# Kernel optimization log

Measured on AMD Instinct MI355X. Metric: run time of the kernel, lower is better.

The kernel has to match this reference:

```python
import jax, jax.numpy as jnp
import numpy as np
from jax import lax

# dims
B, T = 64, 1024
ANNOT, RNN, MEM, ATTN = 512, 1024, 512, 512
FILTERS, KSIZE = 32, 31
PAD = (KSIZE - 1) // 2  # 15, SAME padding


def setup_inputs() -> dict:
    key = jax.random.key(0)
    ks = jax.random.split(key, 20)
    s = 0.02
    return {
        "memory": jax.random.normal(ks[0], (B, MEM), jnp.float32),
        "context": jax.random.normal(ks[1], (B, ANNOT), jnp.float32),
        "rnn_state": jax.random.normal(ks[2], (B, RNN), jnp.float32),
        "annots": jax.random.normal(ks[3], (B, T, ANNOT), jnp.float32),
        "atten": jax.random.uniform(ks[4], (B, 2, T), jnp.float32),
        "mask": jnp.ones((B, T), jnp.int32),
        "t": 0,
        # GRUCell params (torch gate order: r, z, n)
        "W_ih": jax.random.normal(ks[5], (3 * RNN, ANNOT + MEM), jnp.float32) * s,
        "W_hh": jax.random.normal(ks[6], (3 * RNN, RNN), jnp.float32) * s,
        "b_ih": jnp.zeros((3 * RNN,), jnp.float32),
        "b_hh": jnp.zeros((3 * RNN,), jnp.float32),
        # location-sensitive attention params
        "conv_w": jax.random.normal(ks[7], (FILTERS, 2, KSIZE), jnp.float32) * s,
        "loc_w": jax.random.normal(ks[8], (ATTN, FILTERS), jnp.float32) * s,
        "loc_b": jnp.zeros((ATTN,), jnp.float32),
        "q_w": jax.random.normal(ks[9], (ATTN, RNN), jnp.float32) * s,
        "q_b": jnp.zeros((ATTN,), jnp.float32),
        "a_w": jax.random.normal(ks[10], (ATTN, ANNOT), jnp.float32) * s,
        "a_b": jnp.zeros((ATTN,), jnp.float32),
        "v_w": jax.random.normal(ks[11], (1, ATTN), jnp.float32) * s,
    }


def _gru_cell(x, h, W_ih, W_hh, b_ih, b_hh):
    gi = x @ W_ih.T + b_ih  # [B, 3H]
    gh = h @ W_hh.T + b_hh
    i_r, i_z, i_n = jnp.split(gi, 3, axis=-1)
    h_r, h_z, h_n = jnp.split(gh, 3, axis=-1)
    r = jax.nn.sigmoid(i_r + h_r)
    z = jax.nn.sigmoid(i_z + h_z)
    n = jnp.tanh(i_n + r * h_n)
    return (1.0 - z) * n + z * h


def reference(memory, context, rnn_state, annots, atten, mask, t,
              W_ih, W_hh, b_ih, b_hh, conv_w, loc_w, loc_b,
              q_w, q_b, a_w, a_b, v_w):
    # GRU step on [memory; prev_context]
    rnn_input = jnp.concatenate([memory, context], axis=-1)  # [B, MEM+ANNOT]
    rnn_output = _gru_cell(rnn_input, rnn_state, W_ih, W_hh, b_ih, b_hh)  # [B, RNN]

    # location features: SAME conv over [B, 2, T] -> [B, FILTERS, T]
    loc_conv = lax.conv_general_dilated(
        atten, conv_w, window_strides=(1,), padding=[(PAD, PAD)],
        dimension_numbers=("NCH", "OIH", "NCH"))
    processed_loc = jnp.einsum("bft,af->bta", loc_conv, loc_w) + loc_b  # [B,T,ATTN]

    processed_query = (rnn_output @ q_w.T + q_b)[:, None, :]            # [B,1,ATTN]
    processed_annots = jnp.einsum("btd,ad->bta", annots, a_w) + a_b     # [B,T,ATTN]

    energy = jnp.tanh(processed_query + processed_annots + processed_loc)
    alignment = jnp.einsum("bta,a->bt", energy, v_w[0])                 # [B,T]

    # mask fill with -inf where mask == 0
    alignment = jnp.where(mask == 0, -jnp.inf, alignment)

    # sigmoid-normalized attention weights
    sig = jax.nn.sigmoid(alignment)
    alignment = sig / jnp.sum(sig, axis=1, keepdims=True)               # [B,T]

    new_context = jnp.einsum("bt,btd->bd", alignment, annots)           # [B,ANNOT]
    return rnn_output, new_context, alignment
```

## Files before the change

kernel.cpp:

```cpp
#include <hip/hip_runtime.h>

typedef float f32x4 __attribute__((ext_vector_type(4)));
typedef short bf16x8 __attribute__((ext_vector_type(8)));

__device__ __forceinline__ unsigned int pk2(float a, float b) {
    unsigned int ua = __float_as_uint(a); ua += 0x7FFFu + ((ua >> 16) & 1u);
    unsigned int ub = __float_as_uint(b); ub += 0x7FFFu + ((ub >> 16) & 1u);
    return __builtin_amdgcn_perm(ub, ua, 0x07060302u);
}
__device__ __forceinline__ unsigned short bf16_rne(float a) {
    unsigned int ua = __float_as_uint(a);
    ua += 0x7FFFu + ((ua >> 16) & 1u);
    return (unsigned short)(ua >> 16);
}
__device__ __forceinline__ float tanh_fast(float x) {
    float e = __expf(x + x);
    return 1.f - 2.f / (e + 1.f);
}
__device__ __forceinline__ f32x4 mfma16(bf16x8 a, bf16x8 b, f32x4 c) {
    return __builtin_amdgcn_mfma_f32_16x16x32_bf16(a, b, c, 0, 0, 0);
}
__device__ __forceinline__ void ald16(const void* g, void* l) {
    __builtin_amdgcn_global_load_lds(
        (const __attribute__((address_space(1))) unsigned int*)g,
        (__attribute__((address_space(3))) unsigned int*)l, 16, 0, 0);
}

#define Q_WIH   786432
#define Q_WHH   1572864
#define Q_QW    1703936
#define Q_X2    1720320
#define Q_X1    1736704
#define Q_BAW   1802240
#define Q_BLW   1806336
#define Q_EB    1806464
#define NCVT    7057

__global__ __launch_bounds__(256) void k_prep(
    const float* __restrict__ Wih, const float* __restrict__ Whh,
    const float* __restrict__ qw, const float* __restrict__ rnn_state,
    const float* __restrict__ memory, const float* __restrict__ context,
    const float* __restrict__ aw, const float* __restrict__ lw,
    const float* __restrict__ ab, const float* __restrict__ lb,
    const float* __restrict__ atten, const float* __restrict__ convw,
    unsigned short* __restrict__ Wihb, unsigned short* __restrict__ Whhb,
    unsigned short* __restrict__ qwb, unsigned short* __restrict__ X2b,
    unsigned short* __restrict__ X1b, unsigned short* __restrict__ Bbig,
    float* __restrict__ ebias, unsigned short* __restrict__ Lconv)
{
    __shared__ float att_s[2 * 160];
    __shared__ float cw_s[1984];
    const int tid = threadIdx.x;
    if (blockIdx.x < NCVT) {
        int q = blockIdx.x * 256 + tid;
        if (q >= Q_EB) return;
        if (q < Q_WIH) {
            int i = q * 4;
            float4 v = *(const float4*)(Wih + i);
            uint2 u; u.x = pk2(v.x, v.y); u.y = pk2(v.z, v.w);
            *(uint2*)(Wihb + i) = u;
        } else if (q < Q_WHH) {
            int i = (q - Q_WIH) * 4;
            float4 v = *(const float4*)(Whh + i);
            uint2 u; u.x = pk2(v.x, v.y); u.y = pk2(v.z, v.w);
            *(uint2*)(Whhb + i) = u;
        } else if (q < Q_QW) {
            int i = (q - Q_WHH) * 4;
            float4 v = *(const float4*)(qw + i);
            uint2 u; u.x = pk2(v.x, v.y); u.y = pk2(v.z, v.w);
            *(uint2*)(qwb + i) = u;
        } else if (q < Q_X2) {
            int i = (q - Q_QW) * 4;
            float4 v = *(const float4*)(rnn_state + i);
            uint2 u; u.x = pk2(v.x, v.y); u.y = pk2(v.z, v.w);
            *(uint2*)(X2b + i) = u;
        } else if (q < Q_X1) {
            int i = (q - Q_X2) * 4;
            int b = i >> 10, c = i & 1023;
            const float* s = (c < 512) ? (memory + b * 512 + c) : (context + b * 512 + (c - 512));
            float4 v = *(const float4*)s;
            uint2 u; u.x = pk2(v.x, v.y); u.y = pk2(v.z, v.w);
            *(uint2*)(X1b + i) = u;
        } else if (q < Q_BAW) {
            int i = (q - Q_X1) * 4;
            int a = i >> 9, c = i & 511;
            float4 v = *(const float4*)(aw + a * 512 + c);
            uint2 u; u.x = pk2(v.x, v.y); u.y = pk2(v.z, v.w);
            *(uint2*)(Bbig + a * 544 + c) = u;
        } else if (q < Q_BLW) {
            int i = (q - Q_BAW) * 4;
            int a = i >> 5, c = i & 31;
            float4 v = *(const float4*)(lw + a * 32 + c);
            uint2 u; u.x = pk2(v.x, v.y); u.y = pk2(v.z, v.w);
            *(uint2*)(Bbig + a * 544 + 512 + c) = u;
        } else {
            int i = (q - Q_BLW) * 4;
            float4 va = *(const float4*)(ab + i);
            float4 vb = *(const float4*)(lb + i);
            float4 r; r.x = va.x + vb.x; r.y = va.y + vb.y; r.z = va.z + vb.z; r.w = va.w + vb.w;
            *(float4*)(ebias + i) = r;
        }
    } else {
        const int bid = blockIdx.x - NCVT;
        const int b = bid >> 3;
        const int tbase = (bid & 7) * 128;
        for (int i = tid; i < 320; i += 256) {
            int c = i / 160, j = i % 160;
            float v = 0.f;
            int pos = tbase - 15 + j;
            if (j < 158 && pos >= 0 && pos < 1024) v = atten[b * 2048 + c * 1024 + pos];
            att_s[c * 160 + j] = v;
        }
        for (int i = tid; i < 1984; i += 256) cw_s[i] = convw[i];
        __syncthreads();
        const int f = tid & 31, tq = tid >> 5;
        float acc[16];
#pragma unroll
        for (int i = 0; i < 16; ++i) acc[i] = 0.f;
        for (int c = 0; c < 2; ++c) {
            for (int k = 0; k < 31; ++k) {
                float w = cw_s[f * 62 + c * 31 + k];
                int base = c * 160 + tq * 16 + k;
#pragma unroll
                for (int ti = 0; ti < 16; ++ti) acc[ti] += w * att_s[base + ti];
            }
        }
#pragma unroll
        for (int ti = 0; ti < 16; ++ti) {
            int t = tbase + tq * 16 + ti;
            Lconv[(b * 1024 + t) * 32 + f] = bf16_rne(acc[ti]);
        }
    }
}

__global__ __launch_bounds__(256, 4) void k_gemm_ks(
    const unsigned short* __restrict__ A1, const unsigned short* __restrict__ A2,
    const unsigned short* __restrict__ B1, const unsigned short* __restrict__ B2,
    float* __restrict__ C, int N, int nTiles, int n_split, int K, int Klen)
{
    __shared__ __align__(16) unsigned short As[64 * 32];
    __shared__ __align__(16) unsigned short Bs[128 * 32];
    const int tid = threadIdx.x;
    const int nb = blockIdx.x % nTiles;
    const int ks = blockIdx.x / nTiles;
    const int nBase = nb * 128;
    const bool use2 = nBase >= n_split;
    const unsigned short* A = use2 ? A2 : A1;
    const unsigned short* B = use2 ? B2 : B1;
    const int brow0 = nBase - (use2 ? n_split : 0);
    const int lane = tid & 63, w = tid >> 6;
    const int c = lane & 15, qd = lane >> 4;
    const int lr = lane >> 2;
    const int swzl = ((lane & 3) ^ ((lr >> 1) & 3)) * 8;

    const f32x4 fz = {0.f, 0.f, 0.f, 0.f};
    f32x4 acc[4][2];
#pragma unroll
    for (int i = 0; i < 4; ++i) { acc[i][0] = fz; acc[i][1] = fz; }

    const int k0b = ks * Klen;
    const int nkc = Klen >> 5;
    for (int kc = 0; kc < nkc; ++kc) {
        const int k0 = k0b + kc * 32;
        ald16(A + (size_t)(w * 16 + lr) * K + k0 + swzl, &As[w * 512]);
        ald16(B + (size_t)(brow0 + w * 16 + lr) * K + k0 + swzl, &Bs[w * 512]);
        ald16(B + (size_t)(brow0 + 64 + w * 16 + lr) * K + k0 + swzl, &Bs[2048 + w * 512]);
        __syncthreads();
        const int rdoff = (qd ^ ((c >> 1) & 3)) * 8;
        bf16x8 af[4];
#pragma unroll
        for (int i = 0; i < 4; ++i) af[i] = *(const bf16x8*)&As[(i * 16 + c) * 32 + rdoff];
#pragma unroll
        for (int j = 0; j < 2; ++j) {
            bf16x8 bj = *(const bf16x8*)&Bs[(w * 32 + j * 16 + c) * 32 + rdoff];
#pragma unroll
            for (int i = 0; i < 4; ++i) acc[i][j] = mfma16(af[i], bj, acc[i][j]);
        }
        __syncthreads();
    }
    float* Cp = C + (size_t)ks * 64 * N;
#pragma unroll
    for (int i = 0; i < 4; ++i)
#pragma unroll
        for (int r = 0; r < 4; ++r) {
            int row = i * 16 + qd * 4 + r;
#pragma unroll
            for (int j = 0; j < 2; ++j) {
                int col = nBase + w * 32 + j * 16 + c;
                Cp[row * N + col] = acc[i][j][r];
            }
        }
}

__global__ __launch_bounds__(256) void k_gates(
    const float* __restrict__ Cg, const float* __restrict__ h0,
    const float* __restrict__ bih, const float* __restrict__ bhh,
    float* __restrict__ outv, unsigned short* __restrict__ X3b)
{
    int idx = blockIdx.x * 256 + threadIdx.x;
    int b = idx >> 10, h = idx & 1023;
    const float* g0 = Cg + b * 6144;
    const float* g1 = Cg + 393216 + b * 6144;
    float ir = g0[h] + g1[h] + bih[h];
    float iz = g0[h + 1024] + g1[h + 1024] + bih[h + 1024];
    float inn = g0[h + 2048] + g1[h + 2048] + bih[h + 2048];
    float hr = g0[h + 3072] + g1[h + 3072] + bhh[h];
    float hz = g0[h + 4096] + g1[h + 4096] + bhh[h + 1024];
    float hn = g0[h + 5120] + g1[h + 5120] + bhh[h + 2048];
    float r = 1.f / (1.f + __expf(-(ir + hr)));
    float z = 1.f / (1.f + __expf(-(iz + hz)));
    float n = tanh_fast(inn + r * hn);
    float o = (1.f - z) * n + z * h0[idx];
    outv[idx] = o;
    X3b[idx] = bf16_rne(o);
}

__global__ __launch_bounds__(256, 2) void k_attn(
    const float* __restrict__ annots, const unsigned short* __restrict__ Lconv,
    const unsigned short* __restrict__ Bbig, const float* __restrict__ pqP,
    const float* __restrict__ qb, const float* __restrict__ ebias,
    const float* __restrict__ vw, float* __restrict__ wsal)
{
    __shared__ __align__(16) unsigned short As[2][64 * 32];
    __shared__ __align__(16) unsigned short Bs[2][512 * 32];
    __shared__ float red[4][64];
    const int tid = threadIdx.x;
    const int btBase = blockIdx.x * 64;
    const int b = btBase >> 10;
    const int lane = tid & 63, w = tid >> 6;
    const int c = lane & 15, qd = lane >> 4;
    const int lr = lane >> 2;
    const int swzl = ((lane & 3) ^ ((lr >> 1) & 3)) * 8;
    const int arow = tid >> 2, alc = tid & 3;
    const int apofs = (alc ^ ((arow >> 1) & 3)) * 8;

    const f32x4 fz = {0.f, 0.f, 0.f, 0.f};
    f32x4 acc[4][8];
#pragma unroll
    for (int i = 0; i < 4; ++i)
#pragma unroll
        for (int j = 0; j < 8; ++j) acc[i][j] = fz;

    const float* aP = annots + (size_t)(btBase + arow) * 512 + alc * 8;
    const unsigned short* bP = Bbig + (size_t)(w * 16 + lr) * 544 + swzl;

#pragma unroll
    for (int s = 0; s < 8; ++s)
        ald16(bP + (size_t)s * 64 * 544, &Bs[0][s * 2048 + w * 512]);
    {
        float4 v0 = *(const float4*)(aP);
        float4 v1 = *(const float4*)(aP + 4);
        uint4 u;
        u.x = pk2(v0.x, v0.y); u.y = pk2(v0.z, v0.w);
        u.z = pk2(v1.x, v1.y); u.w = pk2(v1.z, v1.w);
        *(uint4*)&As[0][arow * 32 + apofs] = u;
    }
    __syncthreads();

    for (int kc = 0; kc < 17; ++kc) {
        const int cur = kc & 1, nxt = cur ^ 1;
        float4 v0n, v1n;
        if (kc < 16) {
            const int k1 = (kc + 1) * 32;
#pragma unroll
            for (int s = 0; s < 8; ++s)
                ald16(bP + (size_t)s * 64 * 544 + k1, &Bs[nxt][s * 2048 + w * 512]);
            if (kc < 15) {
                v0n = *(const float4*)(aP + k1);
                v1n = *(const float4*)(aP + k1 + 4);
            } else {
                ald16(Lconv + (size_t)(btBase + w * 16 + lr) * 32 + swzl, &As[nxt][w * 512]);
            }
        }
        const int rdoff = (qd ^ ((c >> 1) & 3)) * 8;
        bf16x8 af[4];
#pragma unroll
        for (int i = 0; i < 4; ++i) af[i] = *(const bf16x8*)&As[cur][(i * 16 + c) * 32 + rdoff];
        __builtin_amdgcn_s_setprio(1);
#pragma unroll
        for (int j = 0; j < 8; ++j) {
            bf16x8 bj = *(const bf16x8*)&Bs[cur][(w * 128 + j * 16 + c) * 32 + rdoff];
#pragma unroll
            for (int i = 0; i < 4; ++i) acc[i][j] = mfma16(af[i], bj, acc[i][j]);
        }
        __builtin_amdgcn_s_setprio(0);
        if (kc < 16) {
            if (kc < 15) {
                uint4 u;
                u.x = pk2(v0n.x, v0n.y); u.y = pk2(v0n.z, v0n.w);
                u.z = pk2(v1n.x, v1n.y); u.w = pk2(v1n.z, v1n.w);
                *(uint4*)&As[nxt][arow * 32 + apofs] = u;
            }
            __syncthreads();
        }
    }
    float pe[8], vv[8];
#pragma unroll
    for (int j = 0; j < 8; ++j) {
        int colg = w * 128 + j * 16 + c;
        pe[j] = pqP[b * 512 + colg] + pqP[32768 + b * 512 + colg] + qb[colg] + ebias[colg];
        vv[j] = vw[colg];
    }
#pragma unroll
    for (int i = 0; i < 4; ++i)
#pragma unroll
        for (int r = 0; r < 4; ++r) {
            float p = 0.f;
#pragma unroll
            for (int j = 0; j < 8; ++j)
                p += vv[j] * tanh_fast(acc[i][j][r] + pe[j]);
            p += __shfl_xor(p, 1);
            p += __shfl_xor(p, 2);
            p += __shfl_xor(p, 4);
            p += __shfl_xor(p, 8);
            if (c == 0) red[w][i * 16 + qd * 4 + r] = p;
        }
    __syncthreads();
    if (tid < 64)
        wsal[btBase + tid] = red[0][tid] + red[1][tid] + red[2][tid] + red[3][tid];
}

__global__ __launch_bounds__(256) void k_ctxA(
    const float* __restrict__ annots, const float* __restrict__ wsal,
    const int* __restrict__ mask, float* __restrict__ ctxP)
{
    __shared__ float cx[4][512];
    const int b = blockIdx.x >> 3;
    const int tc = blockIdx.x & 7;
    const int tid = threadIdx.x, lane = tid & 63, wv = tid >> 6;
    const int t0 = tc * 128 + wv * 32;
    const float* wp = wsal + b * 1024;
    const int* mp = mask + b * 1024;
    const float* ap = annots + (size_t)(b * 1024 + t0) * 512 + lane * 4;

    float a0 = 0.f, a1 = 0.f, a2 = 0.f, a3 = 0.f;
    float a4 = 0.f, a5 = 0.f, a6 = 0.f, a7 = 0.f;
#pragma unroll 4
    for (int r = 0; r < 32; ++r) {
        int t = t0 + r;
        float raw = wp[t];
        float s = (mp[t] != 0) ? 1.f / (1.f + __expf(-raw)) : 0.f;
        float4 va = *(const float4*)(ap + (size_t)r * 512);
        float4 vb = *(const float4*)(ap + (size_t)r * 512 + 256);
        a0 += s * va.x; a1 += s * va.y; a2 += s * va.z; a3 += s * va.w;
        a4 += s * vb.x; a5 += s * vb.y; a6 += s * vb.z; a7 += s * vb.w;
    }
    cx[wv][lane * 4 + 0] = a0; cx[wv][lane * 4 + 1] = a1;
    cx[wv][lane * 4 + 2] = a2; cx[wv][lane * 4 + 3] = a3;
    cx[wv][256 + lane * 4 + 0] = a4; cx[wv][256 + lane * 4 + 1] = a5;
    cx[wv][256 + lane * 4 + 2] = a6; cx[wv][256 + lane * 4 + 3] = a7;
    __syncthreads();
    float* cp = ctxP + (size_t)(tc * 64 + b) * 512;
    cp[tid]       = cx[0][tid]       + cx[1][tid]       + cx[2][tid]       + cx[3][tid];
    cp[tid + 256] = cx[0][tid + 256] + cx[1][tid + 256] + cx[2][tid + 256] + cx[3][tid + 256];
}

__global__ __launch_bounds__(256) void k_ctxB(
    const float* __restrict__ wsal, const int* __restrict__ mask,
    const float* __restrict__ ctxP, float* __restrict__ out)
{
    __shared__ float sv[1024];
    __shared__ float wsum[4];
    const int b = blockIdx.x;
    const int tid = threadIdx.x;
    float lsum = 0.f;
#pragma unroll
    for (int p = 0; p < 4; ++p) {
        int t = p * 256 + tid;
        int bt = b * 1024 + t;
        float raw = wsal[bt];
        float s = (mask[bt] != 0) ? 1.f / (1.f + __expf(-raw)) : 0.f;
        sv[t] = s;
        lsum += s;
    }
    for (int off = 32; off > 0; off >>= 1) lsum += __shfl_xor(lsum, off);
    if ((tid & 63) == 0) wsum[tid >> 6] = lsum;
    __syncthreads();
    const float tot = wsum[0] + wsum[1] + wsum[2] + wsum[3];
    const float inv = 1.f / tot;
#pragma unroll
    for (int p = 0; p < 4; ++p) {
        int t = p * 256 + tid;
        out[98304 + b * 1024 + t] = sv[t] * inv;
    }
#pragma unroll
    for (int h = 0; h < 2; ++h) {
        int d = h * 256 + tid;
        float csum = 0.f;
#pragma unroll
        for (int tc = 0; tc < 8; ++tc)
            csum += ctxP[(size_t)(tc * 64 + b) * 512 + d];
        out[65536 + b * 512 + d] = csum * inv;
    }
}

extern "C" void kernel_launch(void* const* d_in, const int* in_sizes, int n_in,
                              void* d_out, int out_size, void* d_ws, size_t ws_size,
                              hipStream_t stream) {
    const float* memory    = (const float*)d_in[0];
    const float* context   = (const float*)d_in[1];
    const float* rnn_state = (const float*)d_in[2];
    const float* annots    = (const float*)d_in[3];
    const float* atten     = (const float*)d_in[4];
    const int*   mask      = (const int*)d_in[5];
    const float* W_ih   = (const float*)d_in[7];
    const float* W_hh   = (const float*)d_in[8];
    const float* b_ih   = (const float*)d_in[9];
    const float* b_hh   = (const float*)d_in[10];
    const float* conv_w = (const float*)d_in[11];
    const float* loc_w  = (const float*)d_in[12];
    const float* loc_b  = (const float*)d_in[13];
    const float* q_w    = (const float*)d_in[14];
    const float* q_b    = (const float*)d_in[15];
    const float* a_w    = (const float*)d_in[16];
    const float* a_b    = (const float*)d_in[17];
    const float* v_w    = (const float*)d_in[18];
    float* out = (float*)d_out;

    char* w8 = (char*)d_ws;
    unsigned short* Lconv = (unsigned short*)(w8 + 0);
    unsigned short* Bbig  = (unsigned short*)(w8 + 4194304);
    unsigned short* Wihb  = (unsigned short*)(w8 + 4751360);
    unsigned short* Whhb  = (unsigned short*)(w8 + 11042816);
    unsigned short* qwb   = (unsigned short*)(w8 + 17334272);
    unsigned short* X1b   = (unsigned short*)(w8 + 18382848);
    unsigned short* X2b   = (unsigned short*)(w8 + 18513920);
    unsigned short* X3b   = (unsigned short*)(w8 + 18644992);
    float*          Cgru  = (float*)(w8 + 18776064);
    float*          pqP   = (float*)(w8 + 18776064);
    float*          ctxP  = (float*)(w8 + 18776064);
    float*          wsal  = (float*)(w8 + 19824640);
    float*          ebias = (float*)(w8 + 21921792);

    k_prep<<<NCVT + 512, 256, 0, stream>>>(W_ih, W_hh, q_w, rnn_state, memory, context,
                                           a_w, loc_w, a_b, loc_b, atten, conv_w,
                                           Wihb, Whhb, qwb, X2b, X1b, Bbig, ebias, Lconv);
    k_gemm_ks<<<96, 256, 0, stream>>>(X1b, X2b, Wihb, Whhb, Cgru, 6144, 48, 3072, 1024, 512);
    k_gates<<<256, 256, 0, stream>>>(Cgru, rnn_state, b_ih, b_hh, out, X3b);
    k_gemm_ks<<<8, 256, 0, stream>>>(X3b, X3b, qwb, qwb, pqP, 512, 4, 0x40000000, 1024, 512);
    k_attn<<<1024, 256, 0, stream>>>(annots, Lconv, Bbig, pqP, q_b, ebias, v_w, wsal);
    k_ctxA<<<512, 256, 0, stream>>>(annots, wsal, mask, ctxP);
    k_ctxB<<<64, 256, 0, stream>>>(wsal, mask, ctxP, out);
}
```

Measured before the change: 345.9 us.

## Fuse context accumulation into attention kernel and widen query GEMM split-K

Removes the separate k_ctxA pass. Each attention block now computes the sigmoid weights for its 64 timesteps and accumulates the weighted annots directly, using the annots tile while it is likely still cached. The partial contexts go to 16 chunks per batch, and k_ctxB reduces over 16 instead of 8. The query GEMM is split into 32 blocks with K chunk 128, and k_attn sums 8 partials. This adds an extra epilogue pass over annots in fp32 and more partial-sum traffic, and ctxP moves to reuse the Wihb workspace region.

```diff
diff --git a/kernel.cpp b/kernel.cpp
--- a/kernel.cpp
+++ b/kernel.cpp
@@ -219,11 +219,13 @@
     const float* __restrict__ annots, const unsigned short* __restrict__ Lconv,
     const unsigned short* __restrict__ Bbig, const float* __restrict__ pqP,
     const float* __restrict__ qb, const float* __restrict__ ebias,
-    const float* __restrict__ vw, float* __restrict__ wsal)
+    const float* __restrict__ vw, const int* __restrict__ mask,
+    float* __restrict__ wsal, float* __restrict__ ctxP)
 {
     __shared__ __align__(16) unsigned short As[2][64 * 32];
     __shared__ __align__(16) unsigned short Bs[2][512 * 32];
     __shared__ float red[4][64];
+    __shared__ float sv[64];
     const int tid = threadIdx.x;
     const int btBase = blockIdx.x * 64;
     const int b = btBase >> 10;
@@ -298,7 +300,10 @@
 #pragma unroll
     for (int j = 0; j < 8; ++j) {
         int colg = w * 128 + j * 16 + c;
-        pe[j] = pqP[b * 512 + colg] + pqP[32768 + b * 512 + colg] + qb[colg] + ebias[colg];
+        float s = qb[colg] + ebias[colg];
+#pragma unroll
+        for (int p = 0; p < 8; ++p) s += pqP[p * 32768 + b * 512 + colg];
+        pe[j] = s;
         vv[j] = vw[colg];
     }
 #pragma unroll
@@ -316,43 +321,37 @@
             if (c == 0) red[w][i * 16 + qd * 4 + r] = p;
         }
     __syncthreads();
-    if (tid < 64)
-        wsal[btBase + tid] = red[0][tid] + red[1][tid] + red[2][tid] + red[3][tid];
-}
-
-__global__ __launch_bounds__(256) void k_ctxA(
-    const float* __restrict__ annots, const float* __restrict__ wsal,
-    const int* __restrict__ mask, float* __restrict__ ctxP)
-{
-    __shared__ float cx[4][512];
-    const int b = blockIdx.x >> 3;
-    const int tc = blockIdx.x & 7;
-    const int tid = threadIdx.x, lane = tid & 63, wv = tid >> 6;
-    const int t0 = tc * 128 + wv * 32;
-    const float* wp = wsal + b * 1024;
-    const int* mp = mask + b * 1024;
-    const float* ap = annots + (size_t)(b * 1024 + t0) * 512 + lane * 4;
-
-    float a0 = 0.f, a1 = 0.f, a2 = 0.f, a3 = 0.f;
-    float a4 = 0.f, a5 = 0.f, a6 = 0.f, a7 = 0.f;
+    if (tid < 64) {
+        float raw = red[0][tid] + red[1][tid] + red[2][tid] + red[3][tid];
+        wsal[btBase + tid] = raw;
+        sv[tid] = (mask[btBase + tid] != 0) ? 1.f / (1.f + __expf(-raw)) : 0.f;
+    }
+    __syncthreads();
+    {
+        float cacc[8];
+#pragma unroll
+        for (int k = 0; k < 8; ++k) cacc[k] = 0.f;
+        const float* ar = annots + (size_t)(btBase + w * 16) * 512 + lane * 8;
 #pragma unroll 4
-    for (int r = 0; r < 32; ++r) {
-        int t = t0 + r;
-        float raw = wp[t];
-        float s = (mp[t] != 0) ? 1.f / (1.f + __expf(-raw)) : 0.f;
-        float4 va = *(const float4*)(ap + (size_t)r * 512);
-        float4 vb = *(const float4*)(ap + (size_t)r * 512 + 256);
-        a0 += s * va.x; a1 += s * va.y; a2 += s * va.z; a3 += s * va.w;
-        a4 += s * vb.x; a5 += s * vb.y; a6 += s * vb.z; a7 += s * vb.w;
-    }
-    cx[wv][lane * 4 + 0] = a0; cx[wv][lane * 4 + 1] = a1;
-    cx[wv][lane * 4 + 2] = a2; cx[wv][lane * 4 + 3] = a3;
-    cx[wv][256 + lane * 4 + 0] = a4; cx[wv][256 + lane * 4 + 1] = a5;
-    cx[wv][256 + lane * 4 + 2] = a6; cx[wv][256 + lane * 4 + 3] = a7;
-    __syncthreads();
-    float* cp = ctxP + (size_t)(tc * 64 + b) * 512;
-    cp[tid]       = cx[0][tid]       + cx[1][tid]       + cx[2][tid]       + cx[3][tid];
-    cp[tid + 256] = cx[0][tid + 256] + cx[1][tid + 256] + cx[2][tid + 256] + cx[3][tid + 256];
+        for (int r2 = 0; r2 < 16; ++r2) {
+            float s = sv[w * 16 + r2];
+            float4 va = *(const float4*)(ar + (size_t)r2 * 512);
+            float4 vb = *(const float4*)(ar + (size_t)r2 * 512 + 4);
+            cacc[0] += s * va.x; cacc[1] += s * va.y;
+            cacc[2] += s * va.z; cacc[3] += s * va.w;
+            cacc[4] += s * vb.x; cacc[5] += s * vb.y;
+            cacc[6] += s * vb.z; cacc[7] += s * vb.w;
+        }
+        float* cxf = (float*)&Bs[0][0];
+#pragma unroll
+        for (int k = 0; k < 8; ++k) cxf[w * 512 + lane * 8 + k] = cacc[k];
+        __syncthreads();
+        const int chunk = blockIdx.x & 15;
+        float* cp = ctxP + ((size_t)chunk * 64 + b) * 512;
+        int d0 = tid * 2;
+        cp[d0]     = cxf[d0]     + cxf[512 + d0]     + cxf[1024 + d0]     + cxf[1536 + d0];
+        cp[d0 + 1] = cxf[d0 + 1] + cxf[512 + d0 + 1] + cxf[1024 + d0 + 1] + cxf[1536 + d0 + 1];
+    }
 }
 
 __global__ __launch_bounds__(256) void k_ctxB(
@@ -388,8 +387,8 @@
         int d = h * 256 + tid;
         float csum = 0.f;
 #pragma unroll
-        for (int tc = 0; tc < 8; ++tc)
-            csum += ctxP[(size_t)(tc * 64 + b) * 512 + d];
+        for (int tc = 0; tc < 16; ++tc)
+            csum += ctxP[((size_t)tc * 64 + b) * 512 + d];
         out[65536 + b * 512 + d] = csum * inv;
     }
 }
@@ -428,7 +427,7 @@
     unsigned short* X3b   = (unsigned short*)(w8 + 18644992);
     float*          Cgru  = (float*)(w8 + 18776064);
     float*          pqP   = (float*)(w8 + 18776064);
-    float*          ctxP  = (float*)(w8 + 18776064);
+    float*          ctxP  = (float*)(w8 + 4751360);
     float*          wsal  = (float*)(w8 + 19824640);
     float*          ebias = (float*)(w8 + 21921792);
 
@@ -437,8 +436,7 @@
                                            Wihb, Whhb, qwb, X2b, X1b, Bbig, ebias, Lconv);
     k_gemm_ks<<<96, 256, 0, stream>>>(X1b, X2b, Wihb, Whhb, Cgru, 6144, 48, 3072, 1024, 512);
     k_gates<<<256, 256, 0, stream>>>(Cgru, rnn_state, b_ih, b_hh, out, X3b);
-    k_gemm_ks<<<8, 256, 0, stream>>>(X3b, X3b, qwb, qwb, pqP, 512, 4, 0x40000000, 1024, 512);
-    k_attn<<<1024, 256, 0, stream>>>(annots, Lconv, Bbig, pqP, q_b, ebias, v_w, wsal);
-    k_ctxA<<<512, 256, 0, stream>>>(annots, wsal, mask, ctxP);
+    k_gemm_ks<<<32, 256, 0, stream>>>(X3b, X3b, qwb, qwb, pqP, 512, 4, 0x40000000, 1024, 128);
+    k_attn<<<1024, 256, 0, stream>>>(annots, Lconv, Bbig, pqP, q_b, ebias, v_w, mask, wsal, ctxP);
     k_ctxB<<<64, 256, 0, stream>>>(wsal, mask, ctxP, out);
 }
```

Measured after the change: 328.4 us, median of 2. 5.1% less time.
